# Performance work log

Hardware: AMD Instinct MI355X
Metric: run time of the kernel (lower is better)

## Reference

```python
import jax, jax.numpy as jnp
import numpy as np

D = 128   # edge_feature_size
E = 128   # number of edges in edge_feature_s_list
B = 4096  # true_batch_size


def setup_inputs() -> dict:
    key = jax.random.key(0)
    k1, k2, k3, k4 = jax.random.split(key, 4)
    temporal_edge_feature = jax.random.normal(k1, (B, D), dtype=jnp.float32)
    edge_feature_s = jax.random.normal(k2, (E, B, D), dtype=jnp.float32)
    W = jax.random.normal(k3, (D, D), dtype=jnp.float32) * (1.0 / np.sqrt(D))
    b = jax.random.normal(k4, (D,), dtype=jnp.float32) * 0.01
    return {
        "true_batch_size": B,
        "temporal_edge_feature": temporal_edge_feature,
        "edge_feature_s": edge_feature_s,
        "W": W,
        "b": b,
    }


def reference(true_batch_size, temporal_edge_feature, edge_feature_s, W, b):
    # Linear projection (same weights applied to source and each edge)
    m_i = temporal_edge_feature @ W.T + b            # [B, D]
    m_j = jnp.einsum('ebd,fd->ebf', edge_feature_s, W) + b  # [E, B, D]
    # Per-(edge, batch) dot-product score
    e_ij = jnp.einsum('bd,ebd->eb', m_i, m_j)        # [E, B]
    # Plain sum-normalization over edges (NOT softmax, faithful to source)
    e_j_sum = jnp.sum(e_ij, axis=0, keepdims=True)   # [1, B]
    weights = e_ij / e_j_sum                         # [E, B]
    # Weighted edge features
    out = weights[:, :, None] * edge_feature_s       # [E, B, D]
    return out
```

## Files before the change

kernel.cpp:

```cpp
#include <hip/hip_runtime.h>

constexpr int D    = 128;
constexpr int E    = 128;
constexpr int BB   = 4096;
constexpr int ROWS = 8;

typedef float f32x4 __attribute__((ext_vector_type(4)));


__global__ __launch_bounds__(128) void gwh_kernel(
    const float* __restrict__ W, const float* __restrict__ bias, float* P)
{
    __shared__ float Wl[D][D];
    __shared__ float bl[D];
    const int t = threadIdx.x;
    const int r = blockIdx.x;

    const float4* W4 = (const float4*)W;
    float4* Wl4 = (float4*)&Wl[0][0];
    for (int i = t; i < D * D / 4; i += 128) Wl4[i] = W4[i];
    bl[t] = bias[t];
    __syncthreads();

    float acc = 0.f;
    for (int k = 0; k < D; ++k) acc += Wl[k][r] * Wl[k][t];
    P[r * D + t] = acc;

    if (r == 0) {
        float hh = 0.f;
        for (int f = 0; f < D; ++f) hh += bl[f] * Wl[f][t];
        P[D * D + t] = hh;
        if (t == 0) {
            float b2 = 0.f;
            for (int f = 0; f < D; ++f) b2 += bl[f] * bl[f];
            P[D * D + D] = b2;
        }
    }
}

__global__ __launch_bounds__(256) void att_fused(
    const float* __restrict__ S, const float* __restrict__ T,
    const float* __restrict__ P, float* out)
{
    const int b  = blockIdx.x;
    const int t  = threadIdx.x;
    const int lc = t & 31;
    const int eb = t >> 5;

    __shared__ float vl[2][D];
    __shared__ float sc[E];
    __shared__ float inv_s, c_s;

    const f32x4* Sp = (const f32x4*)S;

    f32x4 s[16];
    #pragma unroll
    for (int i = 0; i < 16; ++i) {
        const int e = i * 8 + eb;
        s[i] = __builtin_nontemporal_load(Sp + ((size_t)e * BB + b) * 32 + lc);
    }

    {
        const int d  = t & 127;
        const int kh = (t >> 7) * 64;
        const float* Trow = T + (size_t)b * D;
        float acc = 0.f;
        #pragma unroll 8
        for (int kk = 0; kk < 64; ++kk)
            acc += Trow[kh + kk] * P[(size_t)(kh + kk) * D + d];
        vl[t >> 7][d] = acc;
    }
    if (t < 32) {
        const f32x4 t4 = ((const f32x4*)(T + (size_t)b * D))[t];
        const f32x4 h4 = ((const f32x4*)(P + D * D))[t];
        float p = t4.x * h4.x + t4.y * h4.y + t4.z * h4.z + t4.w * h4.w;
        #pragma unroll
        for (int m = 16; m >= 1; m >>= 1) p += __shfl_xor(p, m);
        if (t == 0) c_s = p + P[D * D + D];
    }
    __syncthreads();

    f32x4 v4;
    {
        const f32x4 va = ((const f32x4*)&vl[0][0])[lc];
        const f32x4 vb = ((const f32x4*)&vl[1][0])[lc];
        const f32x4 h4 = ((const f32x4*)(P + D * D))[lc];
        v4 = va + vb + h4;
    }
    const float c = c_s;

    #pragma unroll
    for (int i = 0; i < 16; ++i) {
        float p = s[i].x * v4.x + s[i].y * v4.y + s[i].z * v4.z + s[i].w * v4.w;
        #pragma unroll
        for (int m = 16; m >= 1; m >>= 1) p += __shfl_xor(p, m);
        if (lc == 0) sc[i * 8 + eb] = p + c;
    }
    __syncthreads();

    if (t < 64) {
        double d0 = (double)sc[t] + (double)sc[t + 64];
        #pragma unroll
        for (int m = 32; m >= 1; m >>= 1) d0 += __shfl_xor(d0, m);
        if (t == 0) inv_s = (float)(1.0 / d0);
    }
    __syncthreads();

    const float inv = inv_s;
    f32x4* Op = (f32x4*)out;
    #pragma unroll
    for (int i = 0; i < 16; ++i) {
        const int e = i * 8 + eb;
        const float w = sc[e] * inv;
        __builtin_nontemporal_store(s[i] * w, Op + ((size_t)e * BB + b) * 32 + lc);
    }
}

__global__ __launch_bounds__(256) void prep2_kernel(
    const float* __restrict__ T, const float* __restrict__ P, float* out)
{
    __shared__ float Gl[D][D];
    __shared__ float Tl[ROWS][D];
    __shared__ float hl[D];
    __shared__ float beta_s;

    const int t  = threadIdx.x;
    const int b0 = blockIdx.x * ROWS;

    {
        const float4* Gs = (const float4*)P;
        float4* Gd = (float4*)&Gl[0][0];
        for (int i = t; i < D * D / 4; i += 256) Gd[i] = Gs[i];
        const float4* Ts = (const float4*)(T + (size_t)b0 * D);
        ((float4*)&Tl[0][0])[t] = Ts[t];
        if (t < D) hl[t] = P[D * D + t];
        if (t == 0) beta_s = P[D * D + D];
    }
    __syncthreads();

    const int dc = t & 127;
    const int r0 = (t >> 7) * 4;
    float a0 = hl[dc], a1 = hl[dc], a2 = hl[dc], a3 = hl[dc];
    #pragma unroll 4
    for (int k = 0; k < D; k += 4) {
        const float g0 = Gl[k + 0][dc], g1 = Gl[k + 1][dc],
                    g2 = Gl[k + 2][dc], g3 = Gl[k + 3][dc];
        const float4 t0 = *(const float4*)&Tl[r0 + 0][k];
        const float4 t1 = *(const float4*)&Tl[r0 + 1][k];
        const float4 t2 = *(const float4*)&Tl[r0 + 2][k];
        const float4 t3 = *(const float4*)&Tl[r0 + 3][k];
        a0 += t0.x * g0 + t0.y * g1 + t0.z * g2 + t0.w * g3;
        a1 += t1.x * g0 + t1.y * g1 + t1.z * g2 + t1.w * g3;
        a2 += t2.x * g0 + t2.y * g1 + t2.z * g2 + t2.w * g3;
        a3 += t3.x * g0 + t3.y * g1 + t3.z * g2 + t3.w * g3;
    }
    out[(size_t)(b0 + r0 + 0) * D + dc] = a0;
    out[(size_t)(b0 + r0 + 1) * D + dc] = a1;
    out[(size_t)(b0 + r0 + 2) * D + dc] = a2;
    out[(size_t)(b0 + r0 + 3) * D + dc] = a3;

    const int cr = t >> 5, cl = t & 31;
    const float4 tc = *(const float4*)&Tl[cr][cl * 4];
    const float4 hc = *(const float4*)&hl[cl * 4];
    float p = tc.x * hc.x + tc.y * hc.y + tc.z * hc.z + tc.w * hc.w;
    #pragma unroll
    for (int msk = 16; msk >= 1; msk >>= 1) p += __shfl_xor(p, msk);
    if (cl == 0) out[(size_t)(BB + b0 + cr) * D] = p + beta_s;
}

__global__ __launch_bounds__(256) void att_main(
    const float* __restrict__ S, float* out)
{
    const int b  = blockIdx.x;
    const int t  = threadIdx.x;
    const int lc = t & 31;
    const int eb = t >> 5;

    __shared__ float sc[E];
    __shared__ float inv_s;

    const f32x4* Sp = (const f32x4*)S;
    const f32x4  v4 = ((const f32x4*)(out + (size_t)b * D))[lc];
    const float  c  = out[(size_t)(BB + b) * D];

    f32x4 s[16];
    #pragma unroll
    for (int i = 0; i < 16; ++i) {
        const int e = i * 8 + eb;
        s[i] = __builtin_nontemporal_load(Sp + ((size_t)e * BB + b) * 32 + lc);
    }

    #pragma unroll
    for (int i = 0; i < 16; ++i) {
        float p = s[i].x * v4.x + s[i].y * v4.y + s[i].z * v4.z + s[i].w * v4.w;
        #pragma unroll
        for (int msk = 16; msk >= 1; msk >>= 1) p += __shfl_xor(p, msk);
        if (lc == 0) sc[i * 8 + eb] = p + c;
    }
    __syncthreads();

    if (t < 64) {
        double d0 = (double)sc[t] + (double)sc[t + 64];
        #pragma unroll
        for (int msk = 32; msk >= 1; msk >>= 1) d0 += __shfl_xor(d0, msk);
        if (t == 0) inv_s = (float)(1.0 / d0);
    }
    __syncthreads();

    const float inv = inv_s;
    f32x4* Op = (f32x4*)out;
    #pragma unroll
    for (int i = 0; i < 16; ++i) {
        const int e = i * 8 + eb;
        const float w = sc[e] * inv;
        __builtin_nontemporal_store(s[i] * w, Op + ((size_t)e * BB + b) * 32 + lc);
    }
}

extern "C" void kernel_launch(void* const* d_in, const int* in_sizes, int n_in,
                              void* d_out, int out_size, void* d_ws, size_t ws_size,
                              hipStream_t stream) {
    const float* T    = (const float*)d_in[1];
    const float* S    = (const float*)d_in[2];
    const float* W    = (const float*)d_in[3];
    const float* bias = (const float*)d_in[4];
    float* out        = (float*)d_out;

    const size_t need = (size_t)(D * D + D + 1) * sizeof(float);
    if (d_ws != nullptr && ws_size >= need) {
        float* P = (float*)d_ws;
        gwh_kernel<<<D, D, 0, stream>>>(W, bias, P);
        att_fused<<<BB, 256, 0, stream>>>(S, T, P, out);
    } else {
        float* P = out + (size_t)2 * BB * D;
        gwh_kernel<<<D, D, 0, stream>>>(W, bias, P);
        prep2_kernel<<<BB / ROWS, 256, 0, stream>>>(T, P, out);
        att_main<<<BB, 256, 0, stream>>>(S, out);
    }
}
```

Measured before the change: 465.7 us.

## Process two batch rows per block to amortize the Gram-matrix load

The fused attention kernel now handles two batch indices per block. Each block loads G=WᵀW once and reuses it for both rows' projected vectors. The T·G product is reorganized so each thread does f32x4 loads over a 16-wide k-slice, followed by an 8-way shared-memory reduction. This halves the redundant P reads per batch row but doubles the registers held per thread (32 f32x4 of S), which may lower occupancy for this memory-bound kernel.

Result: no change. 468.2 us (+0.5%).

```diff
diff --git a/kernel.cpp b/kernel.cpp
--- a/kernel.cpp
+++ b/kernel.cpp
@@ -38,81 +38,108 @@
     }
 }
 
-__global__ __launch_bounds__(256) void att_fused(
+__global__ __launch_bounds__(256) void att_fused2(
     const float* __restrict__ S, const float* __restrict__ T,
     const float* __restrict__ P, float* out)
 {
-    const int b  = blockIdx.x;
     const int t  = threadIdx.x;
+    const int b0 = blockIdx.x * 2;
+    const int b1 = b0 + 1;
     const int lc = t & 31;
     const int eb = t >> 5;
 
-    __shared__ float vl[2][D];
-    __shared__ float sc[E];
-    __shared__ float inv_s, c_s;
+    __shared__ float Tl0[D], Tl1[D];
+    __shared__ f32x4 vl0[8][32], vl1[8][32];
+    __shared__ float sc0[E], sc1[E];
+    __shared__ float inv0, inv1, c_s0, c_s1;
 
     const f32x4* Sp = (const f32x4*)S;
 
-    f32x4 s[16];
-    #pragma unroll
-    for (int i = 0; i < 16; ++i) {
-        const int e = i * 8 + eb;
-        s[i] = __builtin_nontemporal_load(Sp + ((size_t)e * BB + b) * 32 + lc);
-    }
+    f32x4 s0[16], s1[16];
+    #pragma unroll
+    for (int i = 0; i < 16; ++i) {
+        const size_t eoff = (size_t)(i * 8 + eb) * BB;
+        s0[i] = __builtin_nontemporal_load(Sp + (eoff + b0) * 32 + lc);
+        s1[i] = __builtin_nontemporal_load(Sp + (eoff + b1) * 32 + lc);
+    }
+
+    if (t < 32)       ((f32x4*)Tl0)[t]      = ((const f32x4*)(T + (size_t)b0 * D))[t];
+    else if (t < 64)  ((f32x4*)Tl1)[t - 32] = ((const f32x4*)(T + (size_t)b1 * D))[t - 32];
+    __syncthreads();
 
     {
-        const int d  = t & 127;
-        const int kh = (t >> 7) * 64;
-        const float* Trow = T + (size_t)b * D;
-        float acc = 0.f;
-        #pragma unroll 8
-        for (int kk = 0; kk < 64; ++kk)
-            acc += Trow[kh + kk] * P[(size_t)(kh + kk) * D + d];
-        vl[t >> 7][d] = acc;
-    }
-    if (t < 32) {
-        const f32x4 t4 = ((const f32x4*)(T + (size_t)b * D))[t];
-        const f32x4 h4 = ((const f32x4*)(P + D * D))[t];
-        float p = t4.x * h4.x + t4.y * h4.y + t4.z * h4.z + t4.w * h4.w;
+        const int dg = t & 31, ks = t >> 5;
+        const f32x4* P4 = (const f32x4*)P;
+        f32x4 a0 = {0.f, 0.f, 0.f, 0.f}, a1 = a0;
+        #pragma unroll
+        for (int kk = 0; kk < 16; ++kk) {
+            const int k = ks * 16 + kk;
+            const f32x4 g4 = P4[(size_t)k * 32 + dg];
+            a0 += Tl0[k] * g4;
+            a1 += Tl1[k] * g4;
+        }
+        vl0[ks][dg] = a0;
+        vl1[ks][dg] = a1;
+    }
+    if (t < 64) {
+        const int cl = t & 31;
+        const float* Trow = (t < 32) ? Tl0 : Tl1;
+        const f32x4 tc = ((const f32x4*)Trow)[cl];
+        const f32x4 hc = ((const f32x4*)(P + D * D))[cl];
+        float p = tc.x * hc.x + tc.y * hc.y + tc.z * hc.z + tc.w * hc.w;
         #pragma unroll
         for (int m = 16; m >= 1; m >>= 1) p += __shfl_xor(p, m);
-        if (t == 0) c_s = p + P[D * D + D];
-    }
-    __syncthreads();
-
-    f32x4 v4;
+        if (t == 0)  c_s0 = p + P[D * D + D];
+        if (t == 32) c_s1 = p + P[D * D + D];
+    }
+    __syncthreads();
+
+    f32x4 v0, v1;
     {
-        const f32x4 va = ((const f32x4*)&vl[0][0])[lc];
-        const f32x4 vb = ((const f32x4*)&vl[1][0])[lc];
         const f32x4 h4 = ((const f32x4*)(P + D * D))[lc];
-        v4 = va + vb + h4;
-    }
-    const float c = c_s;
-
-    #pragma unroll
-    for (int i = 0; i < 16; ++i) {
-        float p = s[i].x * v4.x + s[i].y * v4.y + s[i].z * v4.z + s[i].w * v4.w;
-        #pragma unroll
-        for (int m = 16; m >= 1; m >>= 1) p += __shfl_xor(p, m);
-        if (lc == 0) sc[i * 8 + eb] = p + c;
+        f32x4 r0 = h4, r1 = h4;
+        #pragma unroll
+        for (int ks = 0; ks < 8; ++ks) { r0 += vl0[ks][lc]; r1 += vl1[ks][lc]; }
+        v0 = r0; v1 = r1;
+    }
+    const float cc0 = c_s0, cc1 = c_s1;
+
+    #pragma unroll
+    for (int i = 0; i < 16; ++i) {
+        float p0 = s0[i].x * v0.x + s0[i].y * v0.y + s0[i].z * v0.z + s0[i].w * v0.w;
+        float p1 = s1[i].x * v1.x + s1[i].y * v1.y + s1[i].z * v1.z + s1[i].w * v1.w;
+        #pragma unroll
+        for (int m = 16; m >= 1; m >>= 1) {
+            p0 += __shfl_xor(p0, m);
+            p1 += __shfl_xor(p1, m);
+        }
+        if (lc == 0) { sc0[i * 8 + eb] = p0 + cc0; sc1[i * 8 + eb] = p1 + cc1; }
     }
     __syncthreads();
 
     if (t < 64) {
-        double d0 = (double)sc[t] + (double)sc[t + 64];
+        double d0 = (double)sc0[t] + (double)sc0[t + 64];
         #pragma unroll
         for (int m = 32; m >= 1; m >>= 1) d0 += __shfl_xor(d0, m);
-        if (t == 0) inv_s = (float)(1.0 / d0);
-    }
-    __syncthreads();
-
-    const float inv = inv_s;
+        if (t == 0) inv0 = (float)(1.0 / d0);
+    } else if (t < 128) {
+        const int tl = t - 64;
+        double d1 = (double)sc1[tl] + (double)sc1[tl + 64];
+        #pragma unroll
+        for (int m = 32; m >= 1; m >>= 1) d1 += __shfl_xor(d1, m);
+        if (t == 64) inv1 = (float)(1.0 / d1);
+    }
+    __syncthreads();
+
+    const float i0 = inv0, i1 = inv1;
     f32x4* Op = (f32x4*)out;
     #pragma unroll
     for (int i = 0; i < 16; ++i) {
-        const int e = i * 8 + eb;
-        const float w = sc[e] * inv;
-        __builtin_nontemporal_store(s[i] * w, Op + ((size_t)e * BB + b) * 32 + lc);
+        const size_t eoff = (size_t)(i * 8 + eb) * BB;
+        const float w0 = sc0[i * 8 + eb] * i0;
+        const float w1 = sc1[i * 8 + eb] * i1;
+        __builtin_nontemporal_store(s0[i] * w0, Op + (eoff + b0) * 32 + lc);
+        __builtin_nontemporal_store(s1[i] * w1, Op + (eoff + b1) * 32 + lc);
     }
 }
 
@@ -230,7 +257,7 @@
     if (d_ws != nullptr && ws_size >= need) {
         float* P = (float*)d_ws;
         gwh_kernel<<<D, D, 0, stream>>>(W, bias, P);
-        att_fused<<<BB, 256, 0, stream>>>(S, T, P, out);
+        att_fused2<<<BB / 2, 256, 0, stream>>>(S, T, P, out);
     } else {
         float* P = out + (size_t)2 * BB * D;
         gwh_kernel<<<D, D, 0, stream>>>(W, bias, P);
```
